# Optimization experiments

Measured on AMD Instinct MI355X. Metric: run time of the kernel, lower is better.

The kernel has to match this reference:

```python
import jax, jax.numpy as jnp
import numpy as np

EPS = 1e-8  # torch F.cosine_similarity eps


def setup_inputs() -> dict:
    key = jax.random.key(0)
    B, CAP, CD, CTX = 32, 32768, 64, 64
    ks = jax.random.split(key, 9)
    inp = {
        "query_content": jax.random.normal(ks[0], (B, CD), jnp.float32),
        "query_context": jax.random.normal(ks[1], (B, CTX), jnp.float32),
        "memory_content": 0.1 * jax.random.normal(ks[2], (CAP, CD), jnp.float32),
        "memory_contexts": 0.1 * jax.random.normal(ks[3], (CAP, CTX), jnp.float32),
        "memory_freshness": jnp.ones((CAP,), jnp.float32),
        "W1": jax.random.normal(ks[4], (2 * CD, CD), jnp.float32) / np.sqrt(2 * CD),
        "b1": 0.01 * jax.random.normal(ks[5], (CD,), jnp.float32),
        "W2": jax.random.normal(ks[6], (CD, 1), jnp.float32) / np.sqrt(CD),
        "b2": 0.01 * jax.random.normal(ks[7], (1,), jnp.float32),
        "top_k": 16,
    }
    return inp


def reference(query_content, query_context, memory_content, memory_contexts,
              memory_freshness, W1, b1, W2, b2, top_k):
    B, CD = query_content.shape
    # similarity_calculator MLP over all (query, memory) pairs.
    # Linear on concat([q, m]) == q @ W1[:CD] + m @ W1[CD:]  (avoids the concat).
    q_part = query_content @ W1[:CD]            # [B, CD]
    m_part = memory_content @ W1[CD:]           # [CAP, CD]
    h = jax.nn.relu(q_part[:, None, :] + m_part[None, :, :] + b1)  # [B, CAP, CD]
    content_sim = jax.nn.sigmoid(jnp.einsum('bch,h->bc', h, W2[:, 0]) + b2[0])  # [B, CAP]

    # cosine similarity between query_context and each stored context
    qn = query_context / jnp.maximum(jnp.linalg.norm(query_context, axis=-1, keepdims=True), EPS)
    mn = memory_contexts / jnp.maximum(jnp.linalg.norm(memory_contexts, axis=-1, keepdims=True), EPS)
    context_sim = qn @ mn.T                      # [B, CAP]

    time_weights = memory_freshness              # time_mask is all-ones in source
    final = 0.5 * content_sim + 0.3 * context_sim + 0.2 * time_weights[None, :]

    top_similarities, top_indices = jax.lax.top_k(final, top_k)   # [B, k]
    retrieved_content = memory_content[top_indices]               # [B, k, CD]
    retrieved_time_weights = time_weights[top_indices]            # [B, k]
    return (retrieved_content, top_similarities, retrieved_time_weights)
```

## Files before the change

kernel.cpp:

```cpp
#include <hip/hip_runtime.h>
#include <math.h>

#define CAP   32768
#define NB    32
#define ROWS  64
#define NBLK  (CAP / ROWS)
#define TOPK  16
#define CEPS  1e-8f

#define PITCH 68
#define CHUNK 2048
#define NCHUNK (CAP / CHUNK)

#define WS_QP    0
#define WS_QN    2048
#define WS_FINAL 4096

__global__ __launch_bounds__(64) void prep_kernel(
    const float* __restrict__ qc,
    const float* __restrict__ qctx,
    const float* __restrict__ W1,
    const float* __restrict__ b1,
    float* __restrict__ ws)
{
    const int b = blockIdx.x;
    const int j = threadIdx.x;

    float a0 = b1[j], a1 = 0.f, a2 = 0.f, a3 = 0.f;
    #pragma unroll
    for (int i = 0; i < 64; i += 4) {
        a0 = fmaf(qc[b * 64 + i + 0], W1[(i + 0) * 64 + j], a0);
        a1 = fmaf(qc[b * 64 + i + 1], W1[(i + 1) * 64 + j], a1);
        a2 = fmaf(qc[b * 64 + i + 2], W1[(i + 2) * 64 + j], a2);
        a3 = fmaf(qc[b * 64 + i + 3], W1[(i + 3) * 64 + j], a3);
    }
    ws[WS_QP + b * 64 + j] = (a0 + a1) + (a2 + a3);

    float x = qctx[b * 64 + j];
    float ss = x * x;
    ss += __shfl_xor(ss, 1,  64);
    ss += __shfl_xor(ss, 2,  64);
    ss += __shfl_xor(ss, 4,  64);
    ss += __shfl_xor(ss, 8,  64);
    ss += __shfl_xor(ss, 16, 64);
    ss += __shfl_xor(ss, 32, 64);
    ws[WS_QN + b * 64 + j] = x / fmaxf(sqrtf(ss), CEPS);
}

__global__ __launch_bounds__(256) void score_kernel(
    const float* __restrict__ mcont,
    const float* __restrict__ mctx,
    const float* __restrict__ fresh,
    const float* __restrict__ W1,
    const float* __restrict__ W2,
    const float* __restrict__ b2,
    float* __restrict__ ws)
{
    __shared__ float s_mc[ROWS * PITCH];
    __shared__ float s_qp[NB * PITCH];
    __shared__ float s_qn[NB * PITCH];
    __shared__ float s_base[ROWS];
    __shared__ float s_inv[ROWS];

    const int tid = threadIdx.x;
    const int C0 = blockIdx.x * ROWS;

    const float4* g_mc = (const float4*)(mcont + (size_t)C0 * 64);
    #pragma unroll
    for (int t = tid; t < ROWS * 16; t += 256) {
        int r = t >> 4, c4 = t & 15;
        *(float4*)&s_mc[r * PITCH + c4 * 4] = g_mc[t];
    }
    const float4* g_qp = (const float4*)(ws + WS_QP);
    const float4* g_qn = (const float4*)(ws + WS_QN);
    #pragma unroll
    for (int t = tid; t < NB * 16; t += 256) {
        int r = t >> 4, c4 = t & 15;
        *(float4*)&s_qp[r * PITCH + c4 * 4] = g_qp[t];
        *(float4*)&s_qn[r * PITCH + c4 * 4] = g_qn[t];
    }
    {
        const int r = tid >> 2, q = tid & 3;
        const float* xr = mctx + (size_t)(C0 + r) * 64 + q * 16;
        float ss = 0.f;
        #pragma unroll
        for (int i = 0; i < 4; ++i) {
            float4 x = *(const float4*)&xr[i * 4];
            ss = fmaf(x.x, x.x, ss); ss = fmaf(x.y, x.y, ss);
            ss = fmaf(x.z, x.z, ss); ss = fmaf(x.w, x.w, ss);
        }
        ss += __shfl_xor(ss, 1, 64);
        ss += __shfl_xor(ss, 2, 64);
        if (q == 0) {
            s_inv[r]  = 0.3f / fmaxf(sqrtf(ss), CEPS);
            s_base[r] = 0.2f * fresh[C0 + r];
        }
    }
    __syncthreads();

    const int c_lo = tid & 15;
    const int j0 = (tid >> 4) * 4;
    {
        float acc[4][4] = {{0.f}};
        #pragma unroll 4
        for (int i4 = 0; i4 < 16; ++i4) {
            float4 w0 = *(const float4*)&W1[(64 + i4 * 4 + 0) * 64 + j0];
            float4 w1r = *(const float4*)&W1[(64 + i4 * 4 + 1) * 64 + j0];
            float4 w2r = *(const float4*)&W1[(64 + i4 * 4 + 2) * 64 + j0];
            float4 w3r = *(const float4*)&W1[(64 + i4 * 4 + 3) * 64 + j0];
            #pragma unroll
            for (int ci = 0; ci < 4; ++ci) {
                float4 m = *(const float4*)&s_mc[(c_lo + 16 * ci) * PITCH + i4 * 4];
                acc[ci][0] = fmaf(m.x, w0.x, acc[ci][0]);
                acc[ci][1] = fmaf(m.x, w0.y, acc[ci][1]);
                acc[ci][2] = fmaf(m.x, w0.z, acc[ci][2]);
                acc[ci][3] = fmaf(m.x, w0.w, acc[ci][3]);
                acc[ci][0] = fmaf(m.y, w1r.x, acc[ci][0]);
                acc[ci][1] = fmaf(m.y, w1r.y, acc[ci][1]);
                acc[ci][2] = fmaf(m.y, w1r.z, acc[ci][2]);
                acc[ci][3] = fmaf(m.y, w1r.w, acc[ci][3]);
                acc[ci][0] = fmaf(m.z, w2r.x, acc[ci][0]);
                acc[ci][1] = fmaf(m.z, w2r.y, acc[ci][1]);
                acc[ci][2] = fmaf(m.z, w2r.z, acc[ci][2]);
                acc[ci][3] = fmaf(m.z, w2r.w, acc[ci][3]);
                acc[ci][0] = fmaf(m.w, w3r.x, acc[ci][0]);
                acc[ci][1] = fmaf(m.w, w3r.y, acc[ci][1]);
                acc[ci][2] = fmaf(m.w, w3r.z, acc[ci][2]);
                acc[ci][3] = fmaf(m.w, w3r.w, acc[ci][3]);
            }
        }
        __syncthreads();
        #pragma unroll
        for (int jj = 0; jj < 4; ++jj)
            #pragma unroll
            for (int ci = 0; ci < 4; ++ci)
                s_mc[(j0 + jj) * PITCH + c_lo + 16 * ci] = acc[ci][jj];
    }
    __syncthreads();

    const int bq = (tid & 15) << 1;
    const int cq = (tid >> 4) << 2;
    float4 a1v[2];
    a1v[0] = make_float4(0.f, 0.f, 0.f, 0.f);
    a1v[1] = make_float4(0.f, 0.f, 0.f, 0.f);
    float a2[2][4] = {{0.f}};
    const float* mxb = mctx + (size_t)C0 * 64;

    #pragma unroll 4
    for (int j4 = 0; j4 < 16; ++j4) {
        const int jo = j4 * 4;
        float4 w2v = *(const float4*)(W2 + jo);
        float4 qp0 = *(const float4*)&s_qp[ bq      * PITCH + jo];
        float4 qp1 = *(const float4*)&s_qp[(bq + 1) * PITCH + jo];
        float4 qn0 = *(const float4*)&s_qn[ bq      * PITCH + jo];
        float4 qn1 = *(const float4*)&s_qn[(bq + 1) * PITCH + jo];
        float4 m0 = *(const float4*)&s_mc[(jo + 0) * PITCH + cq];
        float4 m1 = *(const float4*)&s_mc[(jo + 1) * PITCH + cq];
        float4 m2 = *(const float4*)&s_mc[(jo + 2) * PITCH + cq];
        float4 m3 = *(const float4*)&s_mc[(jo + 3) * PITCH + cq];

        #pragma unroll
        for (int bi = 0; bi < 2; ++bi) {
            float4 qp = bi ? qp1 : qp0;
            float4& av = a1v[bi];
            av.x = fmaf(fmaxf(qp.x + m0.x, 0.f), w2v.x, av.x);
            av.y = fmaf(fmaxf(qp.x + m0.y, 0.f), w2v.x, av.y);
            av.z = fmaf(fmaxf(qp.x + m0.z, 0.f), w2v.x, av.z);
            av.w = fmaf(fmaxf(qp.x + m0.w, 0.f), w2v.x, av.w);
            av.x = fmaf(fmaxf(qp.y + m1.x, 0.f), w2v.y, av.x);
            av.y = fmaf(fmaxf(qp.y + m1.y, 0.f), w2v.y, av.y);
            av.z = fmaf(fmaxf(qp.y + m1.z, 0.f), w2v.y, av.z);
            av.w = fmaf(fmaxf(qp.y + m1.w, 0.f), w2v.y, av.w);
            av.x = fmaf(fmaxf(qp.z + m2.x, 0.f), w2v.z, av.x);
            av.y = fmaf(fmaxf(qp.z + m2.y, 0.f), w2v.z, av.y);
            av.z = fmaf(fmaxf(qp.z + m2.z, 0.f), w2v.z, av.z);
            av.w = fmaf(fmaxf(qp.z + m2.w, 0.f), w2v.z, av.w);
            av.x = fmaf(fmaxf(qp.w + m3.x, 0.f), w2v.w, av.x);
            av.y = fmaf(fmaxf(qp.w + m3.y, 0.f), w2v.w, av.y);
            av.z = fmaf(fmaxf(qp.w + m3.z, 0.f), w2v.w, av.z);
            av.w = fmaf(fmaxf(qp.w + m3.w, 0.f), w2v.w, av.w);
        }
        #pragma unroll
        for (int ci = 0; ci < 4; ++ci) {
            float4 xv = *(const float4*)&mxb[(cq + ci) * 64 + jo];
            a2[0][ci] = fmaf(qn0.x, xv.x, a2[0][ci]);
            a2[0][ci] = fmaf(qn0.y, xv.y, a2[0][ci]);
            a2[0][ci] = fmaf(qn0.z, xv.z, a2[0][ci]);
            a2[0][ci] = fmaf(qn0.w, xv.w, a2[0][ci]);
            a2[1][ci] = fmaf(qn1.x, xv.x, a2[1][ci]);
            a2[1][ci] = fmaf(qn1.y, xv.y, a2[1][ci]);
            a2[1][ci] = fmaf(qn1.z, xv.z, a2[1][ci]);
            a2[1][ci] = fmaf(qn1.w, xv.w, a2[1][ci]);
        }
    }

    const float b2v = b2[0];
    float4 inv4  = *(const float4*)&s_inv[cq];
    float4 base4 = *(const float4*)&s_base[cq];
    #pragma unroll
    for (int bi = 0; bi < 2; ++bi) {
        float4 r;
        r.x = 0.5f / (1.f + expf(-(a1v[bi].x + b2v))) + a2[bi][0] * inv4.x + base4.x;
        r.y = 0.5f / (1.f + expf(-(a1v[bi].y + b2v))) + a2[bi][1] * inv4.y + base4.y;
        r.z = 0.5f / (1.f + expf(-(a1v[bi].z + b2v))) + a2[bi][2] * inv4.z + base4.z;
        r.w = 0.5f / (1.f + expf(-(a1v[bi].w + b2v))) + a2[bi][3] * inv4.w + base4.w;
        *(float4*)&ws[WS_FINAL + (size_t)(bq + bi) * CAP + C0 + cq] = r;
    }
}

__global__ __launch_bounds__(1024) void topk_fused(
    const float* __restrict__ mcont,
    const float* __restrict__ fresh,
    const float* __restrict__ ws,
    float* __restrict__ out)
{
    __shared__ float s_val[NCHUNK * TOPK];
    __shared__ int   s_idx[NCHUNK * TOPK];

    const int lane = threadIdx.x & 63;
    const int w    = threadIdx.x >> 6;
    const int b    = blockIdx.x;
    const float* row = ws + WS_FINAL + (size_t)b * CAP;
    const int cbase = w * CHUNK;

    float v[32];
    #pragma unroll
    for (int g = 0; g < 8; ++g) {
        float4 t = *(const float4*)&row[cbase + g * 256 + lane * 4];
        v[4 * g + 0] = t.x; v[4 * g + 1] = t.y;
        v[4 * g + 2] = t.z; v[4 * g + 3] = t.w;
    }

    float outv = 0.f;
    int   outi = 0;

    for (int k = 0; k < TOPK; ++k) {
        float bv = v[0]; int bj = 0;
        #pragma unroll
        for (int j = 1; j < 32; ++j)
            if (v[j] > bv) { bv = v[j]; bj = j; }
        int bi = cbase + (bj >> 2) * 256 + lane * 4 + (bj & 3);

        #pragma unroll
        for (int off = 1; off < 64; off <<= 1) {
            float ov = __shfl_xor(bv, off, 64);
            int   oi = __shfl_xor(bi, off, 64);
            if (ov > bv || (ov == bv && oi < bi)) { bv = ov; bi = oi; }
        }
        if (lane == k) { outv = bv; outi = bi; }

        int rel = bi - cbase;
        bool mine = (((rel >> 2) & 63) == lane);
        int wj = ((rel >> 8) << 2) | (rel & 3);
        #pragma unroll
        for (int j = 0; j < 32; ++j)
            if (mine && wj == j) v[j] = -INFINITY;
    }

    if (lane < TOPK) {
        s_val[w * TOPK + lane] = outv;
        s_idx[w * TOPK + lane] = outi;
    }
    __syncthreads();

    if (w != 0) return;

    float* out_content = out;
    float* out_sim     = out + NB * TOPK * 64;
    float* out_tw      = out + NB * TOPK * 64 + NB * TOPK;

    float mv[4]; int mi[4];
    #pragma unroll
    for (int s = 0; s < 4; ++s) {
        int cand = s * 64 + lane;
        mv[s] = s_val[cand];
        mi[s] = s_idx[cand];
    }

    float wval = 0.f; int widx = 0;
    for (int k = 0; k < TOPK; ++k) {
        float bv = mv[0]; int bi = mi[0];
        #pragma unroll
        for (int s = 1; s < 4; ++s)
            if (mv[s] > bv || (mv[s] == bv && mi[s] < bi)) { bv = mv[s]; bi = mi[s]; }
        #pragma unroll
        for (int off = 1; off < 64; off <<= 1) {
            float ov = __shfl_xor(bv, off, 64);
            int   oi = __shfl_xor(bi, off, 64);
            if (ov > bv || (ov == bv && oi < bi)) { bv = ov; bi = oi; }
        }
        if (lane == k) { wval = bv; widx = bi; }
        #pragma unroll
        for (int s = 0; s < 4; ++s)
            if (mi[s] == bi) mv[s] = -INFINITY;
    }

    if (lane < TOPK) {
        out_sim[b * TOPK + lane] = wval;
        out_tw [b * TOPK + lane] = fresh[widx];
    }

    #pragma unroll
    for (int r = 0; r < TOPK; ++r) {
        int wi = __shfl(widx, r, 64);
        out_content[(size_t)b * TOPK * 64 + r * 64 + lane] =
            mcont[(size_t)wi * 64 + lane];
    }
}

extern "C" void kernel_launch(void* const* d_in, const int* in_sizes, int n_in,
                              void* d_out, int out_size, void* d_ws, size_t ws_size,
                              hipStream_t stream) {
    const float* qc    = (const float*)d_in[0];
    const float* qctx  = (const float*)d_in[1];
    const float* mcont = (const float*)d_in[2];
    const float* mctx  = (const float*)d_in[3];
    const float* fresh = (const float*)d_in[4];
    const float* W1    = (const float*)d_in[5];
    const float* b1    = (const float*)d_in[6];
    const float* W2    = (const float*)d_in[7];
    const float* b2    = (const float*)d_in[8];
    float* out = (float*)d_out;
    float* ws  = (float*)d_ws;

    prep_kernel<<<NB, 64, 0, stream>>>(qc, qctx, W1, b1, ws);
    score_kernel<<<NBLK, 256, 0, stream>>>(mcont, mctx, fresh, W1, W2, b2, ws);
    topk_fused<<<NB, 1024, 0, stream>>>(mcont, fresh, ws, out);
}
```

Before: 141.3 us.

## Split top-k into grid-parallel chunk stage and bitonic merge stage

The single 32-block top-k kernel becomes two kernels. The first runs on a grid of chunks by batch (512 blocks), with each wave selecting a local top-16 from 512 elements, merging the four waves' candidates by a 64-lane bitonic sort, and writing the result back into the score buffer. The second kernel merges the 16 chunk results per row with bitonic sorts and gathers the outputs. This spreads the selection work across many more CUs, at the cost of an extra kernel launch and a global round-trip.

New measurement: 125.9 us. -10.9%, faster.

```diff
diff --git a/kernel.cpp b/kernel.cpp
--- a/kernel.cpp
+++ b/kernel.cpp
@@ -208,101 +208,128 @@
     }
 }
 
-__global__ __launch_bounds__(1024) void topk_fused(
+__device__ __forceinline__ void bitonic64_desc(float& v, int& iv, int lane)
+{
+    #pragma unroll
+    for (int k = 2; k <= 64; k <<= 1) {
+        #pragma unroll
+        for (int j = k >> 1; j > 0; j >>= 1) {
+            float ov = __shfl_xor(v, j, 64);
+            int   oi = __shfl_xor(iv, j, 64);
+            bool low        = (lane & j) == 0;
+            bool dirDesc    = (lane & k) == 0;
+            bool takeBetter = (low == dirDesc);
+            bool otherBetter = (ov > v) || (ov == v && oi < iv);
+            if (otherBetter == takeBetter) { v = ov; iv = oi; }
+        }
+    }
+}
+
+__global__ __launch_bounds__(256) void topk_stage1(float* __restrict__ ws)
+{
+    __shared__ float s_val[64];
+    __shared__ int   s_idx[64];
+
+    const int lane = threadIdx.x & 63;
+    const int w    = threadIdx.x >> 6;
+    const int b    = blockIdx.y;
+    float* row = ws + WS_FINAL + (size_t)b * CAP;
+    const int cbase = blockIdx.x * CHUNK;
+    const int sb = cbase + w * 512;
+
+    float v[8];
+    #pragma unroll
+    for (int g = 0; g < 2; ++g) {
+        float4 t = *(const float4*)&row[sb + g * 256 + lane * 4];
+        v[4 * g + 0] = t.x; v[4 * g + 1] = t.y;
+        v[4 * g + 2] = t.z; v[4 * g + 3] = t.w;
+    }
+
+    float outv = 0.f;
+    int   outi = 0;
+
+    for (int k = 0; k < TOPK; ++k) {
+        float bv = v[0]; int bj = 0;
+        #pragma unroll
+        for (int j = 1; j < 8; ++j)
+            if (v[j] > bv) { bv = v[j]; bj = j; }
+        int bi = sb + (bj >> 2) * 256 + lane * 4 + (bj & 3);
+
+        #pragma unroll
+        for (int off = 1; off < 64; off <<= 1) {
+            float ov = __shfl_xor(bv, off, 64);
+            int   oi = __shfl_xor(bi, off, 64);
+            if (ov > bv || (ov == bv && oi < bi)) { bv = ov; bi = oi; }
+        }
+        if (lane == k) { outv = bv; outi = bi; }
+
+        int rel = bi - sb;
+        bool mine = (((rel >> 2) & 63) == lane);
+        int wj = ((rel >> 8) << 2) | (rel & 3);
+        #pragma unroll
+        for (int j = 0; j < 8; ++j)
+            if (mine && wj == j) v[j] = -INFINITY;
+    }
+
+    if (lane < TOPK) {
+        s_val[w * TOPK + lane] = outv;
+        s_idx[w * TOPK + lane] = outi;
+    }
+    __syncthreads();
+    if (w != 0) return;
+
+    float mv = s_val[lane];
+    int   mi = s_idx[lane];
+    bitonic64_desc(mv, mi, lane);
+    if (lane < TOPK) {
+        row[cbase + lane]        = mv;
+        row[cbase + TOPK + lane] = __int_as_float(mi);
+    }
+}
+
+__global__ __launch_bounds__(256) void topk_stage2(
     const float* __restrict__ mcont,
     const float* __restrict__ fresh,
     const float* __restrict__ ws,
     float* __restrict__ out)
 {
-    __shared__ float s_val[NCHUNK * TOPK];
-    __shared__ int   s_idx[NCHUNK * TOPK];
+    __shared__ float s_val[64];
+    __shared__ int   s_idx[64];
 
     const int lane = threadIdx.x & 63;
     const int w    = threadIdx.x >> 6;
     const int b    = blockIdx.x;
     const float* row = ws + WS_FINAL + (size_t)b * CAP;
-    const int cbase = w * CHUNK;
-
-    float v[32];
-    #pragma unroll
-    for (int g = 0; g < 8; ++g) {
-        float4 t = *(const float4*)&row[cbase + g * 256 + lane * 4];
-        v[4 * g + 0] = t.x; v[4 * g + 1] = t.y;
-        v[4 * g + 2] = t.z; v[4 * g + 3] = t.w;
-    }
-
-    float outv = 0.f;
-    int   outi = 0;
-
-    for (int k = 0; k < TOPK; ++k) {
-        float bv = v[0]; int bj = 0;
-        #pragma unroll
-        for (int j = 1; j < 32; ++j)
-            if (v[j] > bv) { bv = v[j]; bj = j; }
-        int bi = cbase + (bj >> 2) * 256 + lane * 4 + (bj & 3);
-
-        #pragma unroll
-        for (int off = 1; off < 64; off <<= 1) {
-            float ov = __shfl_xor(bv, off, 64);
-            int   oi = __shfl_xor(bi, off, 64);
-            if (ov > bv || (ov == bv && oi < bi)) { bv = ov; bi = oi; }
-        }
-        if (lane == k) { outv = bv; outi = bi; }
-
-        int rel = bi - cbase;
-        bool mine = (((rel >> 2) & 63) == lane);
-        int wj = ((rel >> 8) << 2) | (rel & 3);
-        #pragma unroll
-        for (int j = 0; j < 32; ++j)
-            if (mine && wj == j) v[j] = -INFINITY;
-    }
+
+    const int ch  = w * 4 + (lane >> 4);
+    const int pos = lane & 15;
+    float mv = row[ch * CHUNK + pos];
+    int   mi = __float_as_int(row[ch * CHUNK + TOPK + pos]);
+    bitonic64_desc(mv, mi, lane);
 
     if (lane < TOPK) {
-        s_val[w * TOPK + lane] = outv;
-        s_idx[w * TOPK + lane] = outi;
+        s_val[w * TOPK + lane] = mv;
+        s_idx[w * TOPK + lane] = mi;
     }
     __syncthreads();
-
     if (w != 0) return;
+
+    float fv = s_val[lane];
+    int   fi = s_idx[lane];
+    bitonic64_desc(fv, fi, lane);
 
     float* out_content = out;
     float* out_sim     = out + NB * TOPK * 64;
     float* out_tw      = out + NB * TOPK * 64 + NB * TOPK;
 
-    float mv[4]; int mi[4];
-    #pragma unroll
-    for (int s = 0; s < 4; ++s) {
-        int cand = s * 64 + lane;
-        mv[s] = s_val[cand];
-        mi[s] = s_idx[cand];
-    }
-
-    float wval = 0.f; int widx = 0;
-    for (int k = 0; k < TOPK; ++k) {
-        float bv = mv[0]; int bi = mi[0];
-        #pragma unroll
-        for (int s = 1; s < 4; ++s)
-            if (mv[s] > bv || (mv[s] == bv && mi[s] < bi)) { bv = mv[s]; bi = mi[s]; }
-        #pragma unroll
-        for (int off = 1; off < 64; off <<= 1) {
-            float ov = __shfl_xor(bv, off, 64);
-            int   oi = __shfl_xor(bi, off, 64);
-            if (ov > bv || (ov == bv && oi < bi)) { bv = ov; bi = oi; }
-        }
-        if (lane == k) { wval = bv; widx = bi; }
-        #pragma unroll
-        for (int s = 0; s < 4; ++s)
-            if (mi[s] == bi) mv[s] = -INFINITY;
-    }
-
     if (lane < TOPK) {
-        out_sim[b * TOPK + lane] = wval;
-        out_tw [b * TOPK + lane] = fresh[widx];
+        out_sim[b * TOPK + lane] = fv;
+        out_tw [b * TOPK + lane] = fresh[fi];
     }
 
     #pragma unroll
     for (int r = 0; r < TOPK; ++r) {
-        int wi = __shfl(widx, r, 64);
+        int wi = __shfl(fi, r, 64);
         out_content[(size_t)b * TOPK * 64 + r * 64 + lane] =
             mcont[(size_t)wi * 64 + lane];
     }
@@ -325,5 +352,6 @@
 
     prep_kernel<<<NB, 64, 0, stream>>>(qc, qctx, W1, b1, ws);
     score_kernel<<<NBLK, 256, 0, stream>>>(mcont, mctx, fresh, W1, W2, b2, ws);
-    topk_fused<<<NB, 1024, 0, stream>>>(mcont, fresh, ws, out);
-}
+    topk_stage1<<<dim3(NCHUNK, NB), 256, 0, stream>>>(ws);
+    topk_stage2<<<NB, 256, 0, stream>>>(mcont, fresh, ws, out);
+}
```
